# Performance work log

Measured on AMD Instinct MI355X. Metric: run time of the kernel, lower is better.

Reference implementation:

```python
import jax, jax.numpy as jnp
import numpy as np

NUM_USERS = 100000
NUM_ITEMS = 50000
HIDDEN = 64
NUM_LAYERS = 3
NUM_EDGES = 1200000
N = NUM_USERS + NUM_ITEMS


def setup_inputs() -> dict:
    key = jax.random.key(0)
    k_e, k_u, k_i, k_w, k_b = jax.random.split(key, 5)
    edge_index = jax.random.randint(k_e, (2, NUM_EDGES), 0, N, dtype=jnp.int32)
    users_emb = jax.random.normal(k_u, (NUM_USERS, HIDDEN), dtype=jnp.float32) * 0.01
    items_emb = jax.random.normal(k_i, (NUM_ITEMS, HIDDEN), dtype=jnp.float32) * 0.01
    # GCNConv linear weights (glorot-ish) and zero biases, stacked over layers
    scale = 1.0 / np.sqrt(HIDDEN)
    Ws = jax.random.uniform(k_w, (NUM_LAYERS, HIDDEN, HIDDEN), dtype=jnp.float32,
                            minval=-scale, maxval=scale)
    bs = jnp.zeros((NUM_LAYERS, HIDDEN), dtype=jnp.float32)
    return {"edge_index": edge_index, "users_emb": users_emb,
            "items_emb": items_emb, "Ws": Ws, "bs": bs}


def reference(edge_index, users_emb, items_emb, Ws, bs):
    # GraphSAGEModel.forward: concat user/item embeddings, run num_layers GCNConv
    # (PyG defaults: add self-loops, symmetric D^-1/2 A D^-1/2 normalization, bias).
    x = jnp.concatenate([users_emb, items_emb], axis=0)  # [N, H]

    self_loops = jnp.arange(N, dtype=edge_index.dtype)
    src = jnp.concatenate([edge_index[0], self_loops])  # [E+N]
    dst = jnp.concatenate([edge_index[1], self_loops])

    ones = jnp.ones(src.shape[0], dtype=x.dtype)
    deg = jax.ops.segment_sum(ones, dst, num_segments=N)  # in-degree incl self loop
    dinv = jnp.where(deg > 0, jax.lax.rsqrt(deg), 0.0)
    norm = dinv[src] * dinv[dst]  # [E+N], graph-constant across layers

    for l in range(NUM_LAYERS):
        h = x @ Ws[l]                       # linear transform [N, H]
        msg = h[src] * norm[:, None]        # gather + scale
        x = jax.ops.segment_sum(msg, dst, num_segments=N) + bs[l]
    return (x[:NUM_USERS], users_emb, x[NUM_USERS:], items_emb)
```

## Files before the change

kernel.cpp:

```cpp
#include <hip/hip_runtime.h>
#include <hip/hip_fp16.h>

#define NU 100000
#define NI 50000
#define NN 150000
#define HH 64
#define NE 1200000

#define SCAN_CHUNK 1024
#define NBLK ((NN + SCAN_CHUNK - 1) / SCAN_CHUNK)
#define AGG_BLOCKS (NN / 8)

#define RANK_BLOCKS   ((NE / 16 + 255) / 256)
#define CONCAT4_BLOCKS (NN * 16 / 256)
#define FILL_BLOCKS   ((NE / 8 + 255) / 256)

__global__ __launch_bounds__(256) void k_rank_concat(
    const int4* __restrict__ dst4, int* __restrict__ counts, int4* __restrict__ rank4,
    const float4* __restrict__ users, const float4* __restrict__ items,
    __half2* __restrict__ xs, float4* __restrict__ out,
    __half* __restrict__ pad0, __half* __restrict__ pad1,
    float* __restrict__ dinv, float* __restrict__ p1u) {
    if (blockIdx.x < RANK_BLOCKS) {
        if (blockIdx.x == 0 && threadIdx.x < 18) {
            if (threadIdx.x < 8)       ((int4*)pad0)[threadIdx.x] = make_int4(0, 0, 0, 0);
            else if (threadIdx.x < 16) ((int4*)pad1)[threadIdx.x - 8] = make_int4(0, 0, 0, 0);
            else if (threadIdx.x == 16) dinv[NN] = 0.f;
            else                        p1u[NN] = 0.f;
        }
        int t = blockIdx.x * 256 + threadIdx.x;
        if (t >= NE / 16) return;
        int4 d0 = dst4[4 * t],     d1 = dst4[4 * t + 1];
        int4 d2 = dst4[4 * t + 2], d3 = dst4[4 * t + 3];
        int4 r0, r1, r2, r3;
        r0.x = atomicAdd(&counts[d0.x], 1);
        r0.y = atomicAdd(&counts[d0.y], 1);
        r0.z = atomicAdd(&counts[d0.z], 1);
        r0.w = atomicAdd(&counts[d0.w], 1);
        r1.x = atomicAdd(&counts[d1.x], 1);
        r1.y = atomicAdd(&counts[d1.y], 1);
        r1.z = atomicAdd(&counts[d1.z], 1);
        r1.w = atomicAdd(&counts[d1.w], 1);
        r2.x = atomicAdd(&counts[d2.x], 1);
        r2.y = atomicAdd(&counts[d2.y], 1);
        r2.z = atomicAdd(&counts[d2.z], 1);
        r2.w = atomicAdd(&counts[d2.w], 1);
        r3.x = atomicAdd(&counts[d3.x], 1);
        r3.y = atomicAdd(&counts[d3.y], 1);
        r3.z = atomicAdd(&counts[d3.z], 1);
        r3.w = atomicAdd(&counts[d3.w], 1);
        rank4[4 * t]     = r0;
        rank4[4 * t + 1] = r1;
        rank4[4 * t + 2] = r2;
        rank4[4 * t + 3] = r3;
    } else {
        int i = (blockIdx.x - RANK_BLOCKS) * 256 + threadIdx.x;
        const int UB = NU * 16;
        float4 v;
        if (i < UB) {
            v = users[i];
            out[UB + i] = v;
        } else {
            int j = i - UB;
            v = items[j];
            out[2 * UB + NI * 16 + j] = v;
        }
        xs[2 * i]     = __halves2half2(__float2half_rn(v.x), __float2half_rn(v.y));
        xs[2 * i + 1] = __halves2half2(__float2half_rn(v.z), __float2half_rn(v.w));
    }
}

__global__ __launch_bounds__(256) void k_scan(const int* __restrict__ counts,
                                              float* __restrict__ dinv,
                                              float* __restrict__ dinv2,
                                              int* __restrict__ row_ptr,
                                              unsigned int* __restrict__ state,
                                              const float* __restrict__ Wfull,
                                              const float* __restrict__ bfull,
                                              float* __restrict__ What,
                                              float* __restrict__ cvec) {
    __shared__ float smem[HH * HH];
    __shared__ int s_prefix;
    int t = threadIdx.x;
    int b = blockIdx.x;

    if (b == NBLK) {
        int r = t >> 2, j0 = (t & 3) * 16;
        const float* W0 = Wfull;
        const float* W1 = Wfull + HH * HH;
        const float* W2 = Wfull + 2 * HH * HH;
        float acc[16];
#pragma unroll
        for (int j = 0; j < 16; ++j) acc[j] = 0.f;
        for (int k = 0; k < HH; ++k) {
            float a = W1[r * HH + k];
            const float* bp = W2 + k * HH + j0;
#pragma unroll
            for (int j = 0; j < 16; ++j) acc[j] += a * bp[j];
        }
#pragma unroll
        for (int j = 0; j < 16; ++j) smem[r * HH + j0 + j] = acc[j];
        if (t < HH) {
            float s = 0.f;
            for (int k = 0; k < HH; ++k) s += bfull[HH + k] * W2[k * HH + t];
            cvec[HH + t] = s;
        }
        __syncthreads();
#pragma unroll
        for (int j = 0; j < 16; ++j) acc[j] = 0.f;
        for (int k = 0; k < HH; ++k) {
            float a = W0[r * HH + k];
            const float* bp = smem + k * HH + j0;
#pragma unroll
            for (int j = 0; j < 16; ++j) acc[j] += a * bp[j];
        }
#pragma unroll
        for (int j = 0; j < 16; ++j) What[r * HH + j0 + j] = acc[j];
        if (t < HH) {
            float s = 0.f;
            for (int k = 0; k < HH; ++k) s += bfull[k] * smem[k * HH + t];
            cvec[t] = s;
        }
        return;
    }

    int* sd = (int*)smem;
    int base = b * SCAN_CHUNK + t * 4;
    int c[4];
    if (base + 3 < NN) {
        int4 v = *(const int4*)(counts + base);
        c[0] = v.x; c[1] = v.y; c[2] = v.z; c[3] = v.w;
    } else {
#pragma unroll
        for (int i = 0; i < 4; ++i) c[i] = (base + i < NN) ? counts[base + i] : 0;
    }
#pragma unroll
    for (int i = 0; i < 4; ++i)
        if (base + i < NN) {
            dinv[base + i]  = rsqrtf((float)(c[i] + 1));
            dinv2[base + i] = 1.0f / (float)(c[i] + 1);
        }

    int tt = c[0] + c[1] + c[2] + c[3];
    sd[t] = tt; __syncthreads();
    for (int off = 1; off < 256; off <<= 1) {
        int x = (t >= off) ? sd[t - off] : 0;
        __syncthreads();
        sd[t] += x;
        __syncthreads();
    }

    if (t == 0) {
        unsigned int agg = (unsigned int)sd[255];
        if (b == 0) {
            __hip_atomic_store(&state[0], (2u << 30) | agg, __ATOMIC_RELEASE,
                               __HIP_MEMORY_SCOPE_AGENT);
            s_prefix = 0;
        } else {
            __hip_atomic_store(&state[b], (1u << 30) | agg, __ATOMIC_RELEASE,
                               __HIP_MEMORY_SCOPE_AGENT);
            unsigned int prefix = 0;
            int p = b - 1;
            while (true) {
                unsigned int s = __hip_atomic_load(&state[p], __ATOMIC_ACQUIRE,
                                                   __HIP_MEMORY_SCOPE_AGENT);
                unsigned int fl = s >> 30;
                if (fl == 0u) { __builtin_amdgcn_s_sleep(1); continue; }
                prefix += s & 0x3FFFFFFFu;
                if (fl == 2u) break;
                --p;
            }
            __hip_atomic_store(&state[b], (2u << 30) | (prefix + agg),
                               __ATOMIC_RELEASE, __HIP_MEMORY_SCOPE_AGENT);
            s_prefix = (int)prefix;
        }
    }
    __syncthreads();

    int off0 = s_prefix + (sd[t] - tt);
    int run = 0;
#pragma unroll
    for (int i = 0; i < 4; ++i) {
        if (base + i < NN) row_ptr[base + i] = off0 + run;
        run += c[i];
    }
    if (b == NBLK - 1 && t == 0) row_ptr[NN] = NE;
}

__global__ __launch_bounds__(256) void k_fill(const int4* __restrict__ src4,
                                              const int4* __restrict__ dst4,
                                              const int4* __restrict__ rank4,
                                              const int* __restrict__ row_ptr,
                                              int* __restrict__ col) {
    int t = blockIdx.x * 256 + threadIdx.x;
    if (t >= NE / 8) return;
    int4 s0 = src4[2 * t],  s1 = src4[2 * t + 1];
    int4 d0 = dst4[2 * t],  d1 = dst4[2 * t + 1];
    int4 r0 = rank4[2 * t], r1 = rank4[2 * t + 1];
    int p0 = row_ptr[d0.x], p1 = row_ptr[d0.y], p2 = row_ptr[d0.z], p3 = row_ptr[d0.w];
    int p4 = row_ptr[d1.x], p5 = row_ptr[d1.y], p6 = row_ptr[d1.z], p7 = row_ptr[d1.w];
    col[p0 + r0.x] = s0.x;
    col[p1 + r0.y] = s0.y;
    col[p2 + r0.z] = s0.z;
    col[p3 + r0.w] = s0.w;
    col[p4 + r1.x] = s1.x;
    col[p5 + r1.y] = s1.y;
    col[p6 + r1.z] = s1.z;
    col[p7 + r1.w] = s1.w;
}

template <int UMODE>
__global__ __launch_bounds__(256) void k_aggregate(
    const __half* __restrict__ x, __half* __restrict__ y,
    const float* __restrict__ scale,
    const int* __restrict__ row_ptr, const int* __restrict__ col,
    const float* __restrict__ dinv, const float* __restrict__ pin,
    float* __restrict__ uout, float* __restrict__ pout) {
    int lane = threadIdx.x & 63;
    int wave = blockIdx.x * 4 + (threadIdx.x >> 6);
    int na = wave * 2;
    if (na >= NN) return;
    int nb = na + 1;
    int o  = lane >> 3;
    int f8 = (lane & 7) << 3;

    float a[8], b[8];
#pragma unroll
    for (int j = 0; j < 8; ++j) { a[j] = 0.f; b[j] = 0.f; }
    float ua = 0.f, ub = 0.f;

#define GATHER(r, acc, uacc)                                               \
    {                                                                      \
        int4 raw = *(const int4*)(x + (size_t)(r) * HH + f8);              \
        float dr = 1.f;                                                    \
        if (UMODE) { dr = pin[r]; uacc += dr; }                            \
        __half2* hp = (__half2*)&raw;                                      \
        _Pragma("unroll")                                                  \
        for (int j = 0; j < 4; ++j) {                                      \
            float2 f = __half22float2(hp[j]);                              \
            if (UMODE == 1) { acc[2 * j] += dr * f.x; acc[2 * j + 1] += dr * f.y; } \
            else            { acc[2 * j] += f.x;      acc[2 * j + 1] += f.y; }      \
        }                                                                  \
    }

    int ea = row_ptr[na], enda = row_ptr[na + 1];
    int eb = enda,        endb = row_ptr[nb + 1];

    {
        int ia0 = ea + o - 1, ia1 = ea + o + 7;
        int ib0 = eb + o - 1, ib1 = eb + o + 7;
        int rA0 = (o == 0) ? na : ((ia0 < enda) ? col[ia0] : NN);
        int rA1 = (ia1 < enda) ? col[ia1] : NN;
        int rB0 = (o == 0) ? nb : ((ib0 < endb) ? col[ib0] : NN);
        int rB1 = (ib1 < endb) ? col[ib1] : NN;
        GATHER(rA0, a, ua);
        GATHER(rA1, a, ua);
        GATHER(rB0, b, ub);
        GATHER(rB1, b, ub);
        ea += 15; eb += 15;
    }
    while (ea < enda || eb < endb) {
        int iA0 = ea + o,     iA1 = ea + 8 + o;
        int iB0 = eb + o,     iB1 = eb + 8 + o;
        int rA0 = (iA0 < enda) ? col[iA0] : NN;
        int rA1 = (iA1 < enda) ? col[iA1] : NN;
        int rB0 = (iB0 < endb) ? col[iB0] : NN;
        int rB1 = (iB1 < endb) ? col[iB1] : NN;
        GATHER(rA0, a, ua);
        GATHER(rA1, a, ua);
        GATHER(rB0, b, ub);
        GATHER(rB1, b, ub);
        ea += 16; eb += 16;
    }
#undef GATHER

#pragma unroll
    for (int j = 0; j < 8; ++j) {
        a[j] += __shfl_xor(a[j], 8);  b[j] += __shfl_xor(b[j], 8);
        a[j] += __shfl_xor(a[j], 16); b[j] += __shfl_xor(b[j], 16);
        a[j] += __shfl_xor(a[j], 32); b[j] += __shfl_xor(b[j], 32);
    }
    if (UMODE) {
        ua += __shfl_xor(ua, 8);  ub += __shfl_xor(ub, 8);
        ua += __shfl_xor(ua, 16); ub += __shfl_xor(ub, 16);
        ua += __shfl_xor(ua, 32); ub += __shfl_xor(ub, 32);
    }

    if (o < 2) {
        int   n  = (o == 0) ? na : nb;
        float dv = scale[n];
        __half2 h[4];
#pragma unroll
        for (int j = 0; j < 4; ++j) {
            float x0 = (o == 0) ? a[2 * j]     : b[2 * j];
            float x1 = (o == 0) ? a[2 * j + 1] : b[2 * j + 1];
            h[j] = __halves2half2(__float2half_rn(dv * x0), __float2half_rn(dv * x1));
        }
        *(int4*)(y + (size_t)n * HH + f8) = *(int4*)h;
    }
    if (UMODE && lane < 2) {
        int n = na + lane;
        float s = ((lane == 0) ? ua : ub) * 0.125f;
        float dvn = dinv[n];
        float u = dvn * s;
        uout[n] = u;
        if (UMODE == 1) pout[n] = dvn * u;
    }
}

#define GR 128
#define XSS 65
__global__ __launch_bounds__(256) void k_gemm_final(
    const __half* __restrict__ y, const float* __restrict__ W,
    const float* __restrict__ b2, const float* __restrict__ cvec,
    const float* __restrict__ u1, const float* __restrict__ u2,
    float* __restrict__ out_lo, float* __restrict__ out_hi) {
    __shared__ float xs[GR * XSS];
    __shared__ float ws[HH * HH];
    int t = threadIdx.x;
    int rowBase = blockIdx.x * GR;

    {
        const float4* W4 = (const float4*)W;
        float4* ws4 = (float4*)ws;
#pragma unroll
        for (int i = 0; i < 4; ++i) ws4[i * 256 + t] = W4[i * 256 + t];
    }
#pragma unroll
    for (int it = 0; it < 4; ++it) {
        int g = it * 256 + t;
        int r = g >> 3;
        int c0 = (g & 7) * 8;
        int row = rowBase + r;
        if (row < NN) {
            int4 raw = *(const int4*)(y + (size_t)row * HH + c0);
            __half2 h0 = *(__half2*)&raw.x, h1 = *(__half2*)&raw.y;
            __half2 h2 = *(__half2*)&raw.z, h3 = *(__half2*)&raw.w;
            float2 f0 = __half22float2(h0), f1 = __half22float2(h1);
            float2 f2 = __half22float2(h2), f3 = __half22float2(h3);
            float* dp = xs + r * XSS + c0;
            dp[0] = f0.x; dp[1] = f0.y; dp[2] = f1.x; dp[3] = f1.y;
            dp[4] = f2.x; dp[5] = f2.y; dp[6] = f3.x; dp[7] = f3.y;
        }
    }
    __syncthreads();

    int tx = t & 7;
    int ty = t >> 3;
    int j0 = tx * 8;
    int r0 = ty * 4;

    float acc[4][8];
#pragma unroll
    for (int i = 0; i < 4; ++i)
#pragma unroll
        for (int j = 0; j < 8; ++j) acc[i][j] = 0.f;

    for (int k = 0; k < HH; ++k) {
        float4 w0 = *(const float4*)(ws + k * HH + j0);
        float4 w1 = *(const float4*)(ws + k * HH + j0 + 4);
        float wv[8] = {w0.x, w0.y, w0.z, w0.w, w1.x, w1.y, w1.z, w1.w};
#pragma unroll
        for (int i = 0; i < 4; ++i) {
            float xv = xs[(r0 + i) * XSS + k];
#pragma unroll
            for (int j = 0; j < 8; ++j) acc[i][j] += xv * wv[j];
        }
    }

    float c0j[8], c1j[8], b2j[8];
#pragma unroll
    for (int j = 0; j < 8; ++j) {
        c0j[j] = cvec[j0 + j];
        c1j[j] = cvec[HH + j0 + j];
        b2j[j] = b2[j0 + j];
    }

#pragma unroll
    for (int i = 0; i < 4; ++i) {
        int r = rowBase + r0 + i;
        if (r >= NN) continue;
        float u2r = u2[r], u1r = u1[r];
        float base[8];
#pragma unroll
        for (int j = 0; j < 8; ++j) base[j] = u2r * c0j[j] + u1r * c1j[j] + b2j[j];
        float4 o0 = make_float4(acc[i][0] + base[0], acc[i][1] + base[1],
                                acc[i][2] + base[2], acc[i][3] + base[3]);
        float4 o1 = make_float4(acc[i][4] + base[4], acc[i][5] + base[5],
                                acc[i][6] + base[6], acc[i][7] + base[7]);
        float* d = (r < NU) ? (out_lo + (size_t)r * HH)
                            : (out_hi + (size_t)(r - NU) * HH);
        *(float4*)(d + j0) = o0;
        *(float4*)(d + j0 + 4) = o1;
    }
}

extern "C" void kernel_launch(void* const* d_in, const int* in_sizes, int n_in,
                              void* d_out, int out_size, void* d_ws, size_t ws_size,
                              hipStream_t stream) {
    const int*   edge  = (const int*)d_in[0];
    const int*   src   = edge;
    const int*   dst   = edge + NE;
    const float* users = (const float*)d_in[1];
    const float* items = (const float*)d_in[2];
    const float* Ws    = (const float*)d_in[3];
    const float* bs    = (const float*)d_in[4];
    float*       out   = (float*)d_out;

    char* w = (char*)d_ws;
    __half* Xs0     = (__half*)w; w += (size_t)(NN + 1) * HH * 2;
    __half* Xs1     = (__half*)w; w += (size_t)(NN + 1) * HH * 2;
    float*  dinv    = (float*)w;  w += (size_t)(NN + 1) * 4;
    float*  dinv2   = (float*)w;  w += (size_t)NN * 4;
    float*  u1      = (float*)w;  w += (size_t)NN * 4;
    float*  p1u     = (float*)w;  w += (size_t)(NN + 1) * 4;
    float*  u2      = (float*)w;  w += (size_t)NN * 4;
    float*  What    = (float*)w;  w += (size_t)HH * HH * 4;
    float*  cvec    = (float*)w;  w += (size_t)2 * HH * 4;
    unsigned int* state = (unsigned int*)w; w += 256 * 4;
    int*    counts  = (int*)w;    w += (size_t)NN * 4;
    int*    row_ptr = (int*)w;    w += (size_t)(NN + 1) * 4;
    w += 12;
    int*    col     = (int*)w;    w += (size_t)NE * 4;
    int*    rank    = (int*)w;    w += (size_t)NE * 4;
    (void)ws_size; (void)in_sizes; (void)n_in; (void)out_size;

    hipMemsetAsync(state, 0, (size_t)(256 + NN) * sizeof(int), stream);

    k_rank_concat<<<RANK_BLOCKS + CONCAT4_BLOCKS, 256, 0, stream>>>(
        (const int4*)dst, counts, (int4*)rank,
        (const float4*)users, (const float4*)items, (__half2*)Xs0, (float4*)out,
        Xs0 + (size_t)NN * HH, Xs1 + (size_t)NN * HH, dinv, p1u);
    k_scan<<<NBLK + 1, 256, 0, stream>>>(counts, dinv, dinv2, row_ptr, state,
                                         Ws, bs, What, cvec);
    k_fill<<<FILL_BLOCKS, 256, 0, stream>>>(
        (const int4*)src, (const int4*)dst, (const int4*)rank, row_ptr, col);

    k_aggregate<1><<<AGG_BLOCKS, 256, 0, stream>>>(
        Xs0, Xs1, dinv2, row_ptr, col, dinv, dinv, u1, p1u);
    k_aggregate<2><<<AGG_BLOCKS, 256, 0, stream>>>(
        Xs1, Xs0, dinv2, row_ptr, col, dinv, p1u, u2, nullptr);
    k_aggregate<0><<<AGG_BLOCKS, 256, 0, stream>>>(
        Xs0, Xs1, dinv, row_ptr, col, nullptr, nullptr, nullptr, nullptr);

    const int GEMM_BLOCKS = (NN + GR - 1) / GR;
    k_gemm_final<<<GEMM_BLOCKS, 256, 0, stream>>>(
        Xs1, What, bs + 2 * HH, cvec, u1, u2,
        out , out + (size_t)2 * NU * HH );
}
```

Measured before the change: 388.1 us.

## Fuse scan and CSR fill with grid barrier; aggregate four nodes per wave

Merges the scan kernel and the CSR column fill into one persistent kernel. A software grid barrier (an atomic counter in the state buffer) separates the scan phase from the fill phase, which removes one kernel launch. Separately, each aggregation wave now handles four destination nodes instead of two, giving more independent gathers in flight and a smaller grid, at the cost of more registers (launch bounds set to 256,4). The fill phase now runs on only ~148 blocks in a grid-stride loop, which may cut the parallelism available to the scattered writes.

Result: slower. 446.0 us (+14.9%).

```diff
diff --git a/kernel.cpp b/kernel.cpp
--- a/kernel.cpp
+++ b/kernel.cpp
@@ -9,11 +9,11 @@
 
 #define SCAN_CHUNK 1024
 #define NBLK ((NN + SCAN_CHUNK - 1) / SCAN_CHUNK)
-#define AGG_BLOCKS (NN / 8)
+#define SCAN_GRID (NBLK + 1)
+#define AGG_BLOCKS (NN / 16)
 
 #define RANK_BLOCKS   ((NE / 16 + 255) / 256)
 #define CONCAT4_BLOCKS (NN * 16 / 256)
-#define FILL_BLOCKS   ((NE / 8 + 255) / 256)
 
 __global__ __launch_bounds__(256) void k_rank_concat(
     const int4* __restrict__ dst4, int* __restrict__ counts, int4* __restrict__ rank4,
@@ -70,15 +70,14 @@
     }
 }
 
-__global__ __launch_bounds__(256) void k_scan(const int* __restrict__ counts,
-                                              float* __restrict__ dinv,
-                                              float* __restrict__ dinv2,
-                                              int* __restrict__ row_ptr,
-                                              unsigned int* __restrict__ state,
-                                              const float* __restrict__ Wfull,
-                                              const float* __restrict__ bfull,
-                                              float* __restrict__ What,
-                                              float* __restrict__ cvec) {
+__global__ __launch_bounds__(256) void k_scan_fill(
+    const int* __restrict__ counts,
+    float* __restrict__ dinv, float* __restrict__ dinv2,
+    int* __restrict__ row_ptr, unsigned int* __restrict__ state,
+    const float* __restrict__ Wfull, const float* __restrict__ bfull,
+    float* __restrict__ What, float* __restrict__ cvec,
+    const int4* __restrict__ src4, const int4* __restrict__ dst4,
+    const int4* __restrict__ rank4, int* __restrict__ col) {
     __shared__ float smem[HH * HH];
     __shared__ int s_prefix;
     int t = threadIdx.x;
@@ -121,96 +120,101 @@
             for (int k = 0; k < HH; ++k) s += bfull[k] * smem[k * HH + t];
             cvec[t] = s;
         }
-        return;
-    }
-
-    int* sd = (int*)smem;
-    int base = b * SCAN_CHUNK + t * 4;
-    int c[4];
-    if (base + 3 < NN) {
-        int4 v = *(const int4*)(counts + base);
-        c[0] = v.x; c[1] = v.y; c[2] = v.z; c[3] = v.w;
     } else {
-#pragma unroll
-        for (int i = 0; i < 4; ++i) c[i] = (base + i < NN) ? counts[base + i] : 0;
-    }
-#pragma unroll
-    for (int i = 0; i < 4; ++i)
-        if (base + i < NN) {
-            dinv[base + i]  = rsqrtf((float)(c[i] + 1));
-            dinv2[base + i] = 1.0f / (float)(c[i] + 1);
-        }
-
-    int tt = c[0] + c[1] + c[2] + c[3];
-    sd[t] = tt; __syncthreads();
-    for (int off = 1; off < 256; off <<= 1) {
-        int x = (t >= off) ? sd[t - off] : 0;
+        int* sd = (int*)smem;
+        int base = b * SCAN_CHUNK + t * 4;
+        int c[4];
+        if (base + 3 < NN) {
+            int4 v = *(const int4*)(counts + base);
+            c[0] = v.x; c[1] = v.y; c[2] = v.z; c[3] = v.w;
+        } else {
+#pragma unroll
+            for (int i = 0; i < 4; ++i) c[i] = (base + i < NN) ? counts[base + i] : 0;
+        }
+#pragma unroll
+        for (int i = 0; i < 4; ++i)
+            if (base + i < NN) {
+                dinv[base + i]  = rsqrtf((float)(c[i] + 1));
+                dinv2[base + i] = 1.0f / (float)(c[i] + 1);
+            }
+
+        int tt = c[0] + c[1] + c[2] + c[3];
+        sd[t] = tt; __syncthreads();
+        for (int off = 1; off < 256; off <<= 1) {
+            int x = (t >= off) ? sd[t - off] : 0;
+            __syncthreads();
+            sd[t] += x;
+            __syncthreads();
+        }
+
+        if (t == 0) {
+            unsigned int agg = (unsigned int)sd[255];
+            if (b == 0) {
+                __hip_atomic_store(&state[0], (2u << 30) | agg, __ATOMIC_RELEASE,
+                                   __HIP_MEMORY_SCOPE_AGENT);
+                s_prefix = 0;
+            } else {
+                __hip_atomic_store(&state[b], (1u << 30) | agg, __ATOMIC_RELEASE,
+                                   __HIP_MEMORY_SCOPE_AGENT);
+                unsigned int prefix = 0;
+                int p = b - 1;
+                while (true) {
+                    unsigned int s = __hip_atomic_load(&state[p], __ATOMIC_ACQUIRE,
+                                                       __HIP_MEMORY_SCOPE_AGENT);
+                    unsigned int fl = s >> 30;
+                    if (fl == 0u) { __builtin_amdgcn_s_sleep(1); continue; }
+                    prefix += s & 0x3FFFFFFFu;
+                    if (fl == 2u) break;
+                    --p;
+                }
+                __hip_atomic_store(&state[b], (2u << 30) | (prefix + agg),
+                                   __ATOMIC_RELEASE, __HIP_MEMORY_SCOPE_AGENT);
+                s_prefix = (int)prefix;
+            }
+        }
         __syncthreads();
-        sd[t] += x;
-        __syncthreads();
-    }
-
+
+        int off0 = s_prefix + (sd[t] - tt);
+        int run = 0;
+#pragma unroll
+        for (int i = 0; i < 4; ++i) {
+            if (base + i < NN) row_ptr[base + i] = off0 + run;
+            run += c[i];
+        }
+        if (b == NBLK - 1 && t == 0) row_ptr[NN] = NE;
+    }
+
+    unsigned int* done = state + 192;
+    __threadfence();
+    __syncthreads();
     if (t == 0) {
-        unsigned int agg = (unsigned int)sd[255];
-        if (b == 0) {
-            __hip_atomic_store(&state[0], (2u << 30) | agg, __ATOMIC_RELEASE,
-                               __HIP_MEMORY_SCOPE_AGENT);
-            s_prefix = 0;
-        } else {
-            __hip_atomic_store(&state[b], (1u << 30) | agg, __ATOMIC_RELEASE,
-                               __HIP_MEMORY_SCOPE_AGENT);
-            unsigned int prefix = 0;
-            int p = b - 1;
-            while (true) {
-                unsigned int s = __hip_atomic_load(&state[p], __ATOMIC_ACQUIRE,
-                                                   __HIP_MEMORY_SCOPE_AGENT);
-                unsigned int fl = s >> 30;
-                if (fl == 0u) { __builtin_amdgcn_s_sleep(1); continue; }
-                prefix += s & 0x3FFFFFFFu;
-                if (fl == 2u) break;
-                --p;
-            }
-            __hip_atomic_store(&state[b], (2u << 30) | (prefix + agg),
-                               __ATOMIC_RELEASE, __HIP_MEMORY_SCOPE_AGENT);
-            s_prefix = (int)prefix;
-        }
+        __hip_atomic_fetch_add(done, 1u, __ATOMIC_ACQ_REL, __HIP_MEMORY_SCOPE_AGENT);
+        while (__hip_atomic_load(done, __ATOMIC_ACQUIRE, __HIP_MEMORY_SCOPE_AGENT)
+               < (unsigned int)SCAN_GRID)
+            __builtin_amdgcn_s_sleep(4);
     }
     __syncthreads();
-
-    int off0 = s_prefix + (sd[t] - tt);
-    int run = 0;
-#pragma unroll
-    for (int i = 0; i < 4; ++i) {
-        if (base + i < NN) row_ptr[base + i] = off0 + run;
-        run += c[i];
-    }
-    if (b == NBLK - 1 && t == 0) row_ptr[NN] = NE;
+    __threadfence();
+
+    for (int e = b * 256 + t; e < NE / 8; e += SCAN_GRID * 256) {
+        int4 s0 = src4[2 * e],  s1 = src4[2 * e + 1];
+        int4 d0 = dst4[2 * e],  d1 = dst4[2 * e + 1];
+        int4 r0 = rank4[2 * e], r1 = rank4[2 * e + 1];
+        int p0 = row_ptr[d0.x], p1 = row_ptr[d0.y], p2 = row_ptr[d0.z], p3 = row_ptr[d0.w];
+        int p4 = row_ptr[d1.x], p5 = row_ptr[d1.y], p6 = row_ptr[d1.z], p7 = row_ptr[d1.w];
+        col[p0 + r0.x] = s0.x;
+        col[p1 + r0.y] = s0.y;
+        col[p2 + r0.z] = s0.z;
+        col[p3 + r0.w] = s0.w;
+        col[p4 + r1.x] = s1.x;
+        col[p5 + r1.y] = s1.y;
+        col[p6 + r1.z] = s1.z;
+        col[p7 + r1.w] = s1.w;
+    }
 }
 
-__global__ __launch_bounds__(256) void k_fill(const int4* __restrict__ src4,
-                                              const int4* __restrict__ dst4,
-                                              const int4* __restrict__ rank4,
-                                              const int* __restrict__ row_ptr,
-                                              int* __restrict__ col) {
-    int t = blockIdx.x * 256 + threadIdx.x;
-    if (t >= NE / 8) return;
-    int4 s0 = src4[2 * t],  s1 = src4[2 * t + 1];
-    int4 d0 = dst4[2 * t],  d1 = dst4[2 * t + 1];
-    int4 r0 = rank4[2 * t], r1 = rank4[2 * t + 1];
-    int p0 = row_ptr[d0.x], p1 = row_ptr[d0.y], p2 = row_ptr[d0.z], p3 = row_ptr[d0.w];
-    int p4 = row_ptr[d1.x], p5 = row_ptr[d1.y], p6 = row_ptr[d1.z], p7 = row_ptr[d1.w];
-    col[p0 + r0.x] = s0.x;
-    col[p1 + r0.y] = s0.y;
-    col[p2 + r0.z] = s0.z;
-    col[p3 + r0.w] = s0.w;
-    col[p4 + r1.x] = s1.x;
-    col[p5 + r1.y] = s1.y;
-    col[p6 + r1.z] = s1.z;
-    col[p7 + r1.w] = s1.w;
-}
-
 template <int UMODE>
-__global__ __launch_bounds__(256) void k_aggregate(
+__global__ __launch_bounds__(256, 4) void k_aggregate(
     const __half* __restrict__ x, __half* __restrict__ y,
     const float* __restrict__ scale,
     const int* __restrict__ row_ptr, const int* __restrict__ col,
@@ -218,16 +222,15 @@
     float* __restrict__ uout, float* __restrict__ pout) {
     int lane = threadIdx.x & 63;
     int wave = blockIdx.x * 4 + (threadIdx.x >> 6);
-    int na = wave * 2;
-    if (na >= NN) return;
-    int nb = na + 1;
+    int n0 = wave * 4;
+    if (n0 >= NN) return;
     int o  = lane >> 3;
     int f8 = (lane & 7) << 3;
 
-    float a[8], b[8];
-#pragma unroll
-    for (int j = 0; j < 8; ++j) { a[j] = 0.f; b[j] = 0.f; }
-    float ua = 0.f, ub = 0.f;
+    float a[8], b[8], c[8], d[8];
+#pragma unroll
+    for (int j = 0; j < 8; ++j) { a[j] = 0.f; b[j] = 0.f; c[j] = 0.f; d[j] = 0.f; }
+    float ua = 0.f, ub = 0.f, uc = 0.f, ud = 0.f;
 
 #define GATHER(r, acc, uacc)                                               \
     {                                                                      \
@@ -243,64 +246,97 @@
         }                                                                  \
     }
 
-    int ea = row_ptr[na], enda = row_ptr[na + 1];
-    int eb = enda,        endb = row_ptr[nb + 1];
+    int p0 = row_ptr[n0],     p1 = row_ptr[n0 + 1];
+    int p2 = row_ptr[n0 + 2], p3 = row_ptr[n0 + 3], p4 = row_ptr[n0 + 4];
+    int ea = p0, enda = p1;
+    int eb = p1, endb = p2;
+    int ec = p2, endc = p3;
+    int ed = p3, endd = p4;
 
     {
         int ia0 = ea + o - 1, ia1 = ea + o + 7;
         int ib0 = eb + o - 1, ib1 = eb + o + 7;
-        int rA0 = (o == 0) ? na : ((ia0 < enda) ? col[ia0] : NN);
+        int ic0 = ec + o - 1, ic1 = ec + o + 7;
+        int id0 = ed + o - 1, id1 = ed + o + 7;
+        int rA0 = (o == 0) ? n0     : ((ia0 < enda) ? col[ia0] : NN);
+        int rB0 = (o == 0) ? n0 + 1 : ((ib0 < endb) ? col[ib0] : NN);
+        int rC0 = (o == 0) ? n0 + 2 : ((ic0 < endc) ? col[ic0] : NN);
+        int rD0 = (o == 0) ? n0 + 3 : ((id0 < endd) ? col[id0] : NN);
         int rA1 = (ia1 < enda) ? col[ia1] : NN;
-        int rB0 = (o == 0) ? nb : ((ib0 < endb) ? col[ib0] : NN);
         int rB1 = (ib1 < endb) ? col[ib1] : NN;
+        int rC1 = (ic1 < endc) ? col[ic1] : NN;
+        int rD1 = (id1 < endd) ? col[id1] : NN;
+        GATHER(rA0, a, ua);
+        GATHER(rB0, b, ub);
+        GATHER(rC0, c, uc);
+        GATHER(rD0, d, ud);
+        GATHER(rA1, a, ua);
+        GATHER(rB1, b, ub);
+        GATHER(rC1, c, uc);
+        GATHER(rD1, d, ud);
+        ea += 15; eb += 15; ec += 15; ed += 15;
+    }
+    while (ea < enda || eb < endb || ec < endc || ed < endd) {
+        int iA0 = ea + o, iA1 = ea + 8 + o;
+        int iB0 = eb + o, iB1 = eb + 8 + o;
+        int iC0 = ec + o, iC1 = ec + 8 + o;
+        int iD0 = ed + o, iD1 = ed + 8 + o;
+        int rA0 = (iA0 < enda) ? col[iA0] : NN;
+        int rA1 = (iA1 < enda) ? col[iA1] : NN;
+        int rB0 = (iB0 < endb) ? col[iB0] : NN;
+        int rB1 = (iB1 < endb) ? col[iB1] : NN;
+        int rC0 = (iC0 < endc) ? col[iC0] : NN;
+        int rC1 = (iC1 < endc) ? col[iC1] : NN;
+        int rD0 = (iD0 < endd) ? col[iD0] : NN;
+        int rD1 = (iD1 < endd) ? col[iD1] : NN;
         GATHER(rA0, a, ua);
         GATHER(rA1, a, ua);
         GATHER(rB0, b, ub);
         GATHER(rB1, b, ub);
-        ea += 15; eb += 15;
-    }
-    while (ea < enda || eb < endb) {
-        int iA0 = ea + o,     iA1 = ea + 8 + o;
-        int iB0 = eb + o,     iB1 = eb + 8 + o;
-        int rA0 = (iA0 < enda) ? col[iA0] : NN;
-        int rA1 = (iA1 < enda) ? col[iA1] : NN;
-        int rB0 = (iB0 < endb) ? col[iB0] : NN;
-        int rB1 = (iB1 < endb) ? col[iB1] : NN;
-        GATHER(rA0, a, ua);
-        GATHER(rA1, a, ua);
-        GATHER(rB0, b, ub);
-        GATHER(rB1, b, ub);
-        ea += 16; eb += 16;
+        GATHER(rC0, c, uc);
+        GATHER(rC1, c, uc);
+        GATHER(rD0, d, ud);
+        GATHER(rD1, d, ud);
+        ea += 16; eb += 16; ec += 16; ed += 16;
     }
 #undef GATHER
 
 #pragma unroll
     for (int j = 0; j < 8; ++j) {
         a[j] += __shfl_xor(a[j], 8);  b[j] += __shfl_xor(b[j], 8);
+        c[j] += __shfl_xor(c[j], 8);  d[j] += __shfl_xor(d[j], 8);
         a[j] += __shfl_xor(a[j], 16); b[j] += __shfl_xor(b[j], 16);
+        c[j] += __shfl_xor(c[j], 16); d[j] += __shfl_xor(d[j], 16);
         a[j] += __shfl_xor(a[j], 32); b[j] += __shfl_xor(b[j], 32);
+        c[j] += __shfl_xor(c[j], 32); d[j] += __shfl_xor(d[j], 32);
     }
     if (UMODE) {
         ua += __shfl_xor(ua, 8);  ub += __shfl_xor(ub, 8);
+        uc += __shfl_xor(uc, 8);  ud += __shfl_xor(ud, 8);
         ua += __shfl_xor(ua, 16); ub += __shfl_xor(ub, 16);
+        uc += __shfl_xor(uc, 16); ud += __shfl_xor(ud, 16);
         ua += __shfl_xor(ua, 32); ub += __shfl_xor(ub, 32);
-    }
-
-    if (o < 2) {
-        int   n  = (o == 0) ? na : nb;
+        uc += __shfl_xor(uc, 32); ud += __shfl_xor(ud, 32);
+    }
+
+    if (o < 4) {
+        int   n  = n0 + o;
         float dv = scale[n];
         __half2 h[4];
 #pragma unroll
         for (int j = 0; j < 4; ++j) {
-            float x0 = (o == 0) ? a[2 * j]     : b[2 * j];
-            float x1 = (o == 0) ? a[2 * j + 1] : b[2 * j + 1];
+            float x0 = (o == 0) ? a[2 * j]     : (o == 1) ? b[2 * j]
+                     : (o == 2) ? c[2 * j]     : d[2 * j];
+            float x1 = (o == 0) ? a[2 * j + 1] : (o == 1) ? b[2 * j + 1]
+                     : (o == 2) ? c[2 * j + 1] : d[2 * j + 1];
             h[j] = __halves2half2(__float2half_rn(dv * x0), __float2half_rn(dv * x1));
         }
         *(int4*)(y + (size_t)n * HH + f8) = *(int4*)h;
     }
-    if (UMODE && lane < 2) {
-        int n = na + lane;
-        float s = ((lane == 0) ? ua : ub) * 0.125f;
+    if (UMODE && lane < 4) {
+        int n = n0 + lane;
+        float s = ((lane == 0) ? ua : (lane == 1) ? ub : (lane == 2) ? uc : ud)
+                  * 0.125f;
         float dvn = dinv[n];
         float u = dvn * s;
         uout[n] = u;
@@ -431,10 +467,9 @@
         (const int4*)dst, counts, (int4*)rank,
         (const float4*)users, (const float4*)items, (__half2*)Xs0, (float4*)out,
         Xs0 + (size_t)NN * HH, Xs1 + (size_t)NN * HH, dinv, p1u);
-    k_scan<<<NBLK + 1, 256, 0, stream>>>(counts, dinv, dinv2, row_ptr, state,
-                                         Ws, bs, What, cvec);
-    k_fill<<<FILL_BLOCKS, 256, 0, stream>>>(
-        (const int4*)src, (const int4*)dst, (const int4*)rank, row_ptr, col);
+    k_scan_fill<<<SCAN_GRID, 256, 0, stream>>>(
+        counts, dinv, dinv2, row_ptr, state, Ws, bs, What, cvec,
+        (const int4*)src, (const int4*)dst, (const int4*)rank, col);
 
     k_aggregate<1><<<AGG_BLOCKS, 256, 0, stream>>>(
         Xs0, Xs1, dinv2, row_ptr, col, dinv, dinv, u1, p1u);
```
